# Kernel tuning notes

Hardware: AMD Instinct MI355X
Metric: run time of the kernel (lower is better)

Reference implementation:

```python
import jax, jax.numpy as jnp
import numpy as np

N_ACTIVE = 200000   # active voxels
GRID = 96           # spatial grid extent per axis
C = 128             # inplanes == outplanes
EPS = 1e-4          # scn BatchNormalization default eps


def _build_rulebook(n, g, seed=0):
    """Submanifold 3x3x3 rulebook: for each of 27 offsets, pairs (in_site, out_site)
    where coord[in] = coord[out] + offset and both sites are active. Padded to
    length n with dummy index n."""
    rng = np.random.default_rng(seed)
    lin = rng.choice(g ** 3, size=n, replace=False)
    coords = np.stack(np.unravel_index(lin, (g, g, g)), axis=1)  # [n,3]
    lut = -np.ones(g ** 3, dtype=np.int64)
    lut[lin] = np.arange(n)
    in_rows, out_rows = [], []
    for dx in (-1, 0, 1):
        for dy in (-1, 0, 1):
            for dz in (-1, 0, 1):
                nb = coords + np.array([dx, dy, dz])
                valid = np.all((nb >= 0) & (nb < g), axis=1)
                j = np.full(n, -1, dtype=np.int64)
                j[valid] = lut[np.ravel_multi_index(nb[valid].T, (g, g, g))]
                hit = j >= 0
                ii = j[hit]
                oi = np.nonzero(hit)[0].astype(np.int64)
                pad = n - ii.shape[0]
                in_rows.append(np.concatenate([ii, np.full(pad, n, dtype=np.int64)]))
                out_rows.append(np.concatenate([oi, np.full(pad, n, dtype=np.int64)]))
    return np.stack(in_rows), np.stack(out_rows)  # each [27, n]


def setup_inputs() -> dict:
    key = jax.random.key(0)
    k_feat, k_w1, k_w2 = jax.random.split(key, 3)
    in_idx_np, out_idx_np = _build_rulebook(N_ACTIVE, GRID)
    w_std = 1.0 / np.sqrt(27 * C)
    return {
        "features": jax.random.normal(k_feat, (N_ACTIVE, C), dtype=jnp.float32),
        "W1": jax.random.normal(k_w1, (27, C, C), dtype=jnp.float32) * w_std,
        "gamma1": jnp.ones((C,), jnp.float32),
        "beta1": jnp.zeros((C,), jnp.float32),
        "W2": jax.random.normal(k_w2, (27, C, C), dtype=jnp.float32) * w_std,
        "gamma2": jnp.ones((C,), jnp.float32),
        "beta2": jnp.zeros((C,), jnp.float32),
        "in_idx": jnp.asarray(in_idx_np),
        "out_idx": jnp.asarray(out_idx_np),
    }


def _subm_conv(feats, W, in_idx, out_idx):
    # feats: [N, Cin]; W: [27, Cin, Cout]; rulebook idx: [27, K] (dummy = N)
    n, c_in = feats.shape
    c_out = W.shape[-1]
    feats_pad = jnp.concatenate([feats, jnp.zeros((1, c_in), feats.dtype)], axis=0)

    def step(acc, t):
        ii, oi, w = t
        contrib = feats_pad[ii] @ w  # [K, Cout] gather -> GEMM
        return acc.at[oi].add(contrib), None  # scatter-add (dummy row n absorbs pad)

    acc0 = jnp.zeros((n + 1, c_out), feats.dtype)
    acc, _ = jax.lax.scan(step, acc0, (in_idx, out_idx, W))
    return acc[:n]


def _bn(x, gamma, beta):
    # batch-norm over active sites (training-mode batch stats)
    m = x.mean(axis=0)
    v = x.var(axis=0)
    return (x - m) * jax.lax.rsqrt(v + EPS) * gamma + beta


def reference(features, W1, gamma1, beta1, W2, gamma2, beta2, in_idx, out_idx):
    out = _subm_conv(features, W1, in_idx, out_idx)
    out = jax.nn.relu(_bn(out, gamma1, beta1))          # scn.BatchNormReLU
    out = _subm_conv(out, W2, in_idx, out_idx)
    out = _bn(out, gamma2, beta2)                       # scn.BatchNormalization
    return jax.nn.relu(out + features)                  # AddTable + ReLU
```

## Files before the change

### kernel.cpp

```cpp
#include <hip/hip_runtime.h>

#define NACT 200000
#define MPAD 200064
#define NBLK 1563
#define KOFF 27

typedef __bf16 bf16x8 __attribute__((ext_vector_type(8)));
typedef __bf16 bf16x4 __attribute__((ext_vector_type(4)));
typedef float f32x4 __attribute__((ext_vector_type(4)));

__device__ __forceinline__ void async_load16(const void* g, void* l) {
  __builtin_amdgcn_global_load_lds(
      (__attribute__((address_space(1))) void*)g,
      (__attribute__((address_space(3))) void*)l, 16, 0, 0);
}

__global__ void fill_g(int* __restrict__ G, float* __restrict__ st) {
  int i = blockIdx.x * 256 + threadIdx.x;
  if (i < KOFF * MPAD) G[i] = NACT;
  if (i < 1024) st[i] = 0.f;
}

__global__ void scatter_g(const int* __restrict__ ii, const int* __restrict__ oi,
                          int* __restrict__ G) {
  int i = blockIdx.x * 256 + threadIdx.x;
  if (i >= KOFF * NACT) return;
  int k = i / NACT;
  int o = oi[i];
  G[k * MPAD + o] = ii[i];
}

__global__ void cast_feats(const float* __restrict__ F, __bf16* __restrict__ X) {
  int i = blockIdx.x * 256 + threadIdx.x;
  if (i >= (NACT + 1) * 32) return;
  float4 v = (i < NACT * 32) ? ((const float4*)F)[i] : make_float4(0.f, 0.f, 0.f, 0.f);
  bf16x4 o = {(__bf16)v.x, (__bf16)v.y, (__bf16)v.z, (__bf16)v.w};
  *(bf16x4*)(X + (i << 2)) = o;
}

__global__ void prep_w(const float* __restrict__ W1, const float* __restrict__ W2,
                       __bf16* __restrict__ T1, __bf16* __restrict__ T2) {
  int i = blockIdx.x * 256 + threadIdx.x;
  if (i >= KOFF * 128 * 128) return;
  int k = i >> 14, rem = i & 16383, n = rem >> 7, c = rem & 127;
  int src = (k << 14) + (c << 7) + n;
  T1[i] = (__bf16)W1[src];
  T2[i] = (__bf16)W2[src];
}

__global__ __launch_bounds__(256, 2) void gemm_gather(
    const __bf16* __restrict__ X,
    const __bf16* __restrict__ WT,
    const int* __restrict__ G,
    float* __restrict__ Y)
{
  __shared__ __bf16 Alds[128 * 64];
  __shared__ __bf16 Blds[128 * 64];
  const int t = threadIdx.x;
  const int lane = t & 63;
  const int w = t >> 6;
  const int wm = (w & 1) << 6;
  const int wn = (w >> 1) << 6;
  const int m_base = blockIdx.x << 7;
  const int r0 = t >> 3;
  const int scb = t & 7;
  const int l15 = lane & 15;
  const int q4 = lane >> 4;

  f32x4 acc[4][4];
#pragma unroll
  for (int i = 0; i < 4; ++i)
#pragma unroll
    for (int j = 0; j < 4; ++j) acc[i][j] = (f32x4){0.f, 0.f, 0.f, 0.f};

  for (int kk = 0; kk < KOFF; ++kk) {
    int rowA[4];
#pragma unroll
    for (int j = 0; j < 4; ++j)
      rowA[j] = G[kk * MPAD + m_base + r0 + j * 32];
    const __bf16* wb = WT + (kk << 14);
#pragma unroll
    for (int s = 0; s < 2; ++s) {
      const int c0 = s << 6;
      __syncthreads();
#pragma unroll
      for (int j = 0; j < 4; ++j) {
        const int r = r0 + j * 32;
        const int gcb = scb ^ (r & 7);
        async_load16(wb + (r << 7) + c0 + (gcb << 3), &Blds[(((r << 3) + scb) << 3)]);
        async_load16(X + (rowA[j] << 7) + c0 + (gcb << 3), &Alds[(((r << 3) + scb) << 3)]);
      }
      __syncthreads();
#pragma unroll
      for (int ks = 0; ks < 2; ++ks) {
        bf16x8 af[4], bfr[4];
        const int cb0 = (ks << 2) + q4;
#pragma unroll
        for (int mi = 0; mi < 4; ++mi) {
          const int r = wm + mi * 16 + l15;
          af[mi] = *(const bf16x8*)&Alds[(((r << 3) + (cb0 ^ (r & 7))) << 3)];
        }
#pragma unroll
        for (int ni = 0; ni < 4; ++ni) {
          const int r = wn + ni * 16 + l15;
          bfr[ni] = *(const bf16x8*)&Blds[(((r << 3) + (cb0 ^ (r & 7))) << 3)];
        }
#pragma unroll
        for (int mi = 0; mi < 4; ++mi)
#pragma unroll
          for (int ni = 0; ni < 4; ++ni)
            acc[mi][ni] = __builtin_amdgcn_mfma_f32_16x16x32_bf16(
                af[mi], bfr[ni], acc[mi][ni], 0, 0, 0);
      }
    }
  }
#pragma unroll
  for (int mi = 0; mi < 4; ++mi) {
#pragma unroll
    for (int ni = 0; ni < 4; ++ni) {
      const int col = wn + ni * 16 + l15;
#pragma unroll
      for (int rg = 0; rg < 4; ++rg) {
        const int row = m_base + wm + mi * 16 + (q4 << 2) + rg;
        Y[(row << 7) + col] = acc[mi][ni][rg];
      }
    }
  }
}

__global__ void reduce_stats(const float* __restrict__ Y, float* __restrict__ st) {
  int c = threadIdx.x;
  float s = 0.f, s2 = 0.f;
  for (int r = blockIdx.x; r < NACT; r += gridDim.x) {
    float v = Y[(r << 7) + c];
    s += v; s2 += v * v;
  }
  atomicAdd(&st[c], s);
  atomicAdd(&st[128 + c], s2);
}

__global__ void bn_coeffs(const float* __restrict__ st, const float* __restrict__ gamma,
                          const float* __restrict__ beta, float* __restrict__ co) {
  int c = threadIdx.x;
  float m = st[c] * (1.f / NACT);
  float v = st[128 + c] * (1.f / NACT) - m * m;
  float sc = gamma[c] * rsqrtf(v + 1e-4f);
  co[c] = sc;
  co[128 + c] = beta[c] - m * sc;
}

__global__ void bn_relu_cast(const float* __restrict__ Y, const float* __restrict__ co,
                             __bf16* __restrict__ X2) {
  int i = blockIdx.x * 256 + threadIdx.x;
  if (i >= (NACT + 1) * 32) return;
  bf16x4 o;
  if (i < NACT * 32) {
    int cg = (i & 31) << 2;
    float4 v = ((const float4*)Y)[i];
    float a = fmaxf(fmaf(v.x, co[cg + 0], co[128 + cg + 0]), 0.f);
    float b = fmaxf(fmaf(v.y, co[cg + 1], co[128 + cg + 1]), 0.f);
    float d = fmaxf(fmaf(v.z, co[cg + 2], co[128 + cg + 2]), 0.f);
    float e = fmaxf(fmaf(v.w, co[cg + 3], co[128 + cg + 3]), 0.f);
    o = (bf16x4){(__bf16)a, (__bf16)b, (__bf16)d, (__bf16)e};
  } else {
    o = (bf16x4){(__bf16)0.f, (__bf16)0.f, (__bf16)0.f, (__bf16)0.f};
  }
  *(bf16x4*)(X2 + (i << 2)) = o;
}

__global__ void bn_add_relu(const float* __restrict__ Y, const float* __restrict__ co,
                            const float* __restrict__ F, float* __restrict__ O) {
  int i = blockIdx.x * 256 + threadIdx.x;
  if (i >= NACT * 32) return;
  int cg = (i & 31) << 2;
  float4 v = ((const float4*)Y)[i];
  float4 f = ((const float4*)F)[i];
  float4 o;
  o.x = fmaxf(fmaf(v.x, co[cg + 0], co[128 + cg + 0]) + f.x, 0.f);
  o.y = fmaxf(fmaf(v.y, co[cg + 1], co[128 + cg + 1]) + f.y, 0.f);
  o.z = fmaxf(fmaf(v.z, co[cg + 2], co[128 + cg + 2]) + f.z, 0.f);
  o.w = fmaxf(fmaf(v.w, co[cg + 3], co[128 + cg + 3]) + f.w, 0.f);
  ((float4*)O)[i] = o;
}

extern "C" void kernel_launch(void* const* d_in, const int* in_sizes, int n_in,
                              void* d_out, int out_size, void* d_ws, size_t ws_size,
                              hipStream_t stream) {
  const float* features = (const float*)d_in[0];
  const float* W1       = (const float*)d_in[1];
  const float* gamma1   = (const float*)d_in[2];
  const float* beta1    = (const float*)d_in[3];
  const float* W2       = (const float*)d_in[4];
  const float* gamma2   = (const float*)d_in[5];
  const float* beta2    = (const float*)d_in[6];
  const int* in_idx     = (const int*)d_in[7];
  const int* out_idx    = (const int*)d_in[8];

  char* ws = (char*)d_ws;
  size_t off = 0;
  int*    G  = (int*)(ws + off);    off += (size_t)KOFF * MPAD * 4;
  __bf16* X1 = (__bf16*)(ws + off); off += (size_t)(NACT + 1) * 128 * 2;
  __bf16* X2 = (__bf16*)(ws + off); off += (size_t)(NACT + 1) * 128 * 2;
  __bf16* T1 = (__bf16*)(ws + off); off += (size_t)KOFF * 128 * 128 * 2;
  __bf16* T2 = (__bf16*)(ws + off); off += (size_t)KOFF * 128 * 128 * 2;
  float*  Y  = (float*)(ws + off);  off += (size_t)MPAD * 128 * 4;
  float*  st = (float*)(ws + off);  off += 4096;

  fill_g<<<(KOFF * MPAD + 255) / 256, 256, 0, stream>>>(G, st);
  scatter_g<<<(KOFF * NACT + 255) / 256, 256, 0, stream>>>(in_idx, out_idx, G);
  cast_feats<<<((NACT + 1) * 32 + 255) / 256, 256, 0, stream>>>(features, X1);
  prep_w<<<(KOFF * 128 * 128 + 255) / 256, 256, 0, stream>>>(W1, W2, T1, T2);

  gemm_gather<<<NBLK, 256, 0, stream>>>(X1, T1, G, Y);
  reduce_stats<<<1024, 128, 0, stream>>>(Y, st);
  bn_coeffs<<<1, 128, 0, stream>>>(st, gamma1, beta1, st + 512);
  bn_relu_cast<<<((NACT + 1) * 32 + 255) / 256, 256, 0, stream>>>(Y, st + 512, X2);

  gemm_gather<<<NBLK, 256, 0, stream>>>(X2, T2, G, Y);
  reduce_stats<<<1024, 128, 0, stream>>>(Y, st + 256);
  bn_coeffs<<<1, 128, 0, stream>>>(st + 256, gamma2, beta2, st + 768);
  bn_add_relu<<<(NACT * 32 + 255) / 256, 256, 0, stream>>>(Y, st + 768, features, (float*)d_out);
}
```

Baseline: 758.0 us.

## Fuse BN statistics into gather-GEMM epilogue and store conv output as bf16

```diff
diff --git a/kernel.cpp b/kernel.cpp
--- a/kernel.cpp
+++ b/kernel.cpp
@@ -15,10 +15,9 @@
       (__attribute__((address_space(3))) void*)l, 16, 0, 0);
 }
 
-__global__ void fill_g(int* __restrict__ G, float* __restrict__ st) {
+__global__ void fill_g(int* __restrict__ G) {
   int i = blockIdx.x * 256 + threadIdx.x;
   if (i < KOFF * MPAD) G[i] = NACT;
-  if (i < 1024) st[i] = 0.f;
 }
 
 __global__ void scatter_g(const int* __restrict__ ii, const int* __restrict__ oi,
@@ -28,6 +27,11 @@
   int k = i / NACT;
   int o = oi[i];
   G[k * MPAD + o] = ii[i];
+}
+
+__global__ void fix_g(int* __restrict__ G) {
+  int k = threadIdx.x;
+  if (k < KOFF) G[k * MPAD + NACT] = NACT;
 }
 
 __global__ void cast_feats(const float* __restrict__ F, __bf16* __restrict__ X) {
@@ -48,11 +52,12 @@
   T2[i] = (__bf16)W2[src];
 }
 
-__global__ __launch_bounds__(256, 2) void gemm_gather(
+__global__ __launch_bounds__(256, 4) void gemm_gather(
     const __bf16* __restrict__ X,
     const __bf16* __restrict__ WT,
     const int* __restrict__ G,
-    float* __restrict__ Y)
+    __bf16* __restrict__ Y,
+    float* __restrict__ Pst)
 {
   __shared__ __bf16 Alds[128 * 64];
   __shared__ __bf16 Blds[128 * 64];
@@ -114,6 +119,7 @@
       }
     }
   }
+
 #pragma unroll
   for (int mi = 0; mi < 4; ++mi) {
 #pragma unroll
@@ -122,21 +128,58 @@
 #pragma unroll
       for (int rg = 0; rg < 4; ++rg) {
         const int row = m_base + wm + mi * 16 + (q4 << 2) + rg;
-        Y[(row << 7) + col] = acc[mi][ni][rg];
-      }
-    }
-  }
-}
-
-__global__ void reduce_stats(const float* __restrict__ Y, float* __restrict__ st) {
-  int c = threadIdx.x;
-  float s = 0.f, s2 = 0.f;
-  for (int r = blockIdx.x; r < NACT; r += gridDim.x) {
-    float v = Y[(r << 7) + c];
-    s += v; s2 += v * v;
-  }
-  atomicAdd(&st[c], s);
-  atomicAdd(&st[128 + c], s2);
+        Y[(row << 7) + col] = (__bf16)acc[mi][ni][rg];
+      }
+    }
+  }
+
+  float s[4], s2[4];
+#pragma unroll
+  for (int ni = 0; ni < 4; ++ni) {
+    float a = 0.f, b = 0.f;
+#pragma unroll
+    for (int mi = 0; mi < 4; ++mi)
+#pragma unroll
+      for (int rg = 0; rg < 4; ++rg) {
+        float v = acc[mi][ni][rg];
+        a += v; b += v * v;
+      }
+    s[ni] = a; s2[ni] = b;
+  }
+#pragma unroll
+  for (int ni = 0; ni < 4; ++ni) {
+    s[ni]  += __shfl_xor(s[ni], 16);  s[ni]  += __shfl_xor(s[ni], 32);
+    s2[ni] += __shfl_xor(s2[ni], 16); s2[ni] += __shfl_xor(s2[ni], 32);
+  }
+  float* sc = (float*)Alds;
+  __syncthreads();
+  if (q4 == 0) {
+#pragma unroll
+    for (int ni = 0; ni < 4; ++ni) {
+      sc[(w << 6) + ni * 16 + l15]       = s[ni];
+      sc[256 + (w << 6) + ni * 16 + l15] = s2[ni];
+    }
+  }
+  __syncthreads();
+  {
+    const int kind = t >> 7, col = t & 127;
+    const int w1 = (col >> 6) << 1;
+    const float v = sc[kind * 256 + (w1 << 6) + (col & 63)] +
+                    sc[kind * 256 + ((w1 + 1) << 6) + (col & 63)];
+    Pst[(size_t)t * NBLK + blockIdx.x] = v;
+  }
+}
+
+__global__ void stats_reduce(const float* __restrict__ P, float* __restrict__ st) {
+  int b = blockIdx.x;
+  const float* p = P + (size_t)b * NBLK;
+  float s = 0.f;
+  for (int i = threadIdx.x; i < NBLK; i += 256) s += p[i];
+  for (int off = 32; off; off >>= 1) s += __shfl_down(s, off);
+  __shared__ float ls[4];
+  if ((threadIdx.x & 63) == 0) ls[threadIdx.x >> 6] = s;
+  __syncthreads();
+  if (threadIdx.x == 0) st[b] = ls[0] + ls[1] + ls[2] + ls[3];
 }
 
 __global__ void bn_coeffs(const float* __restrict__ st, const float* __restrict__ gamma,
@@ -149,38 +192,45 @@
   co[128 + c] = beta[c] - m * sc;
 }
 
-__global__ void bn_relu_cast(const float* __restrict__ Y, const float* __restrict__ co,
+__global__ void bn_relu_cast(const __bf16* __restrict__ Y, const float* __restrict__ co,
                              __bf16* __restrict__ X2) {
   int i = blockIdx.x * 256 + threadIdx.x;
-  if (i >= (NACT + 1) * 32) return;
-  bf16x4 o;
-  if (i < NACT * 32) {
-    int cg = (i & 31) << 2;
-    float4 v = ((const float4*)Y)[i];
-    float a = fmaxf(fmaf(v.x, co[cg + 0], co[128 + cg + 0]), 0.f);
-    float b = fmaxf(fmaf(v.y, co[cg + 1], co[128 + cg + 1]), 0.f);
-    float d = fmaxf(fmaf(v.z, co[cg + 2], co[128 + cg + 2]), 0.f);
-    float e = fmaxf(fmaf(v.w, co[cg + 3], co[128 + cg + 3]), 0.f);
-    o = (bf16x4){(__bf16)a, (__bf16)b, (__bf16)d, (__bf16)e};
+  if (i >= (NACT + 1) * 16) return;
+  bf16x8 o;
+  if (i < NACT * 16) {
+    bf16x8 v = ((const bf16x8*)Y)[i];
+    int cg = (i & 15) << 3;
+#pragma unroll
+    for (int e = 0; e < 8; ++e) {
+      float x = fmaf((float)v[e], co[cg + e], co[128 + cg + e]);
+      o[e] = (__bf16)fmaxf(x, 0.f);
+    }
   } else {
-    o = (bf16x4){(__bf16)0.f, (__bf16)0.f, (__bf16)0.f, (__bf16)0.f};
-  }
-  *(bf16x4*)(X2 + (i << 2)) = o;
-}
-
-__global__ void bn_add_relu(const float* __restrict__ Y, const float* __restrict__ co,
+#pragma unroll
+    for (int e = 0; e < 8; ++e) o[e] = (__bf16)0.f;
+  }
+  ((bf16x8*)X2)[i] = o;
+}
+
+__global__ void bn_add_relu(const __bf16* __restrict__ Y, const float* __restrict__ co,
                             const float* __restrict__ F, float* __restrict__ O) {
   int i = blockIdx.x * 256 + threadIdx.x;
-  if (i >= NACT * 32) return;
-  int cg = (i & 31) << 2;
-  float4 v = ((const float4*)Y)[i];
-  float4 f = ((const float4*)F)[i];
-  float4 o;
-  o.x = fmaxf(fmaf(v.x, co[cg + 0], co[128 + cg + 0]) + f.x, 0.f);
-  o.y = fmaxf(fmaf(v.y, co[cg + 1], co[128 + cg + 1]) + f.y, 0.f);
-  o.z = fmaxf(fmaf(v.z, co[cg + 2], co[128 + cg + 2]) + f.z, 0.f);
-  o.w = fmaxf(fmaf(v.w, co[cg + 3], co[128 + cg + 3]) + f.w, 0.f);
-  ((float4*)O)[i] = o;
+  if (i >= NACT * 16) return;
+  bf16x8 v = ((const bf16x8*)Y)[i];
+  float4 f0 = ((const float4*)F)[2 * i];
+  float4 f1 = ((const float4*)F)[2 * i + 1];
+  int cg = (i & 15) << 3;
+  float4 o0, o1;
+  o0.x = fmaxf(fmaf((float)v[0], co[cg + 0], co[128 + cg + 0]) + f0.x, 0.f);
+  o0.y = fmaxf(fmaf((float)v[1], co[cg + 1], co[128 + cg + 1]) + f0.y, 0.f);
+  o0.z = fmaxf(fmaf((float)v[2], co[cg + 2], co[128 + cg + 2]) + f0.z, 0.f);
+  o0.w = fmaxf(fmaf((float)v[3], co[cg + 3], co[128 + cg + 3]) + f0.w, 0.f);
+  o1.x = fmaxf(fmaf((float)v[4], co[cg + 4], co[128 + cg + 4]) + f1.x, 0.f);
+  o1.y = fmaxf(fmaf((float)v[5], co[cg + 5], co[128 + cg + 5]) + f1.y, 0.f);
+  o1.z = fmaxf(fmaf((float)v[6], co[cg + 6], co[128 + cg + 6]) + f1.z, 0.f);
+  o1.w = fmaxf(fmaf((float)v[7], co[cg + 7], co[128 + cg + 7]) + f1.w, 0.f);
+  ((float4*)O)[2 * i] = o0;
+  ((float4*)O)[2 * i + 1] = o1;
 }
 
 extern "C" void kernel_launch(void* const* d_in, const int* in_sizes, int n_in,
@@ -198,26 +248,27 @@
 
   char* ws = (char*)d_ws;
   size_t off = 0;
-  int*    G  = (int*)(ws + off);    off += (size_t)KOFF * MPAD * 4;
-  __bf16* X1 = (__bf16*)(ws + off); off += (size_t)(NACT + 1) * 128 * 2;
-  __bf16* X2 = (__bf16*)(ws + off); off += (size_t)(NACT + 1) * 128 * 2;
-  __bf16* T1 = (__bf16*)(ws + off); off += (size_t)KOFF * 128 * 128 * 2;
-  __bf16* T2 = (__bf16*)(ws + off); off += (size_t)KOFF * 128 * 128 * 2;
-  float*  Y  = (float*)(ws + off);  off += (size_t)MPAD * 128 * 4;
-  float*  st = (float*)(ws + off);  off += 4096;
-
-  fill_g<<<(KOFF * MPAD + 255) / 256, 256, 0, stream>>>(G, st);
+  int*    G   = (int*)(ws + off);    off += (size_t)KOFF * MPAD * 4;
+  __bf16* X   = (__bf16*)(ws + off); off += (size_t)(NACT + 1) * 128 * 2;
+  __bf16* T1  = (__bf16*)(ws + off); off += (size_t)KOFF * 128 * 128 * 2;
+  __bf16* T2  = (__bf16*)(ws + off); off += (size_t)KOFF * 128 * 128 * 2;
+  __bf16* Y   = (__bf16*)(ws + off); off += (size_t)MPAD * 128 * 2;
+  float*  Pst = (float*)(ws + off);  off += (size_t)256 * NBLK * 4;
+  float*  st  = (float*)(ws + off);  off += 4096;
+
+  fill_g<<<(KOFF * MPAD + 255) / 256, 256, 0, stream>>>(G);
   scatter_g<<<(KOFF * NACT + 255) / 256, 256, 0, stream>>>(in_idx, out_idx, G);
-  cast_feats<<<((NACT + 1) * 32 + 255) / 256, 256, 0, stream>>>(features, X1);
+  fix_g<<<1, 32, 0, stream>>>(G);
+  cast_feats<<<((NACT + 1) * 32 + 255) / 256, 256, 0, stream>>>(features, X);
   prep_w<<<(KOFF * 128 * 128 + 255) / 256, 256, 0, stream>>>(W1, W2, T1, T2);
 
-  gemm_gather<<<NBLK, 256, 0, stream>>>(X1, T1, G, Y);
-  reduce_stats<<<1024, 128, 0, stream>>>(Y, st);
+  gemm_gather<<<NBLK, 256, 0, stream>>>(X, T1, G, Y, Pst);
+  stats_reduce<<<256, 256, 0, stream>>>(Pst, st);
   bn_coeffs<<<1, 128, 0, stream>>>(st, gamma1, beta1, st + 512);
-  bn_relu_cast<<<((NACT + 1) * 32 + 255) / 256, 256, 0, stream>>>(Y, st + 512, X2);
-
-  gemm_gather<<<NBLK, 256, 0, stream>>>(X2, T2, G, Y);
-  reduce_stats<<<1024, 128, 0, stream>>>(Y, st + 256);
-  bn_coeffs<<<1, 128, 0, stream>>>(st + 256, gamma2, beta2, st + 768);
-  bn_add_relu<<<(NACT * 32 + 255) / 256, 256, 0, stream>>>(Y, st + 768, features, (float*)d_out);
-}
+  bn_relu_cast<<<((NACT + 1) * 16 + 255) / 256, 256, 0, stream>>>(Y, st + 512, X);
+
+  gemm_gather<<<NBLK, 256, 0, stream>>>(X, T2, G, Y, Pst);
+  stats_reduce<<<256, 256, 0, stream>>>(Pst, st);
+  bn_coeffs<<<1, 128, 0, stream>>>(st, gamma2, beta2, st + 768);
+  bn_add_relu<<<(NACT * 16 + 255) / 256, 256, 0, stream>>>(Y, st + 768, features, (float*)d_out);
+}
```

Measured after the change: 609.9 us. -19.5%, faster.
